# Optimization experiments

Measured on AMD Instinct MI355X. Metric: run time of the kernel, lower is better.

## Reference

```python
import jax, jax.numpy as jnp
import numpy as np

B, N = 32, 200000          # images, flattened candidates per image (anchors*classes)
NUM_CLASSES = 21           # VOC-style class count for the label-offset trick
CONF_THR = 0.05            # cfg.PRED_CONF_THR
NMS_THR = 0.5              # cfg.PRED_NMS_THR
TOPK = 500                 # cfg.PRED_SELECT_TOPK
KEEP_MAX = 100             # cfg.PRED_NMS_KEEP


def setup_inputs() -> dict:
    key = jax.random.key(0)
    k1, k2, k3, k4 = jax.random.split(key, 4)
    pscores = jax.random.uniform(k1, (B, N), dtype=jnp.float32)
    # well-formed ltrb boxes in [0,1]: right>left, bottom>top
    xy1 = jax.random.uniform(k2, (B, N, 2), dtype=jnp.float32) * 0.8
    wh = jax.random.uniform(k3, (B, N, 2), dtype=jnp.float32) * 0.2 + 0.01
    pboxes = jnp.concatenate([xy1, xy1 + wh], axis=-1)
    plabels = jax.random.randint(k4, (B, N), 0, NUM_CLASSES)
    return {"pscores": pscores, "pboxes": pboxes, "plabels": plabels}


def _box_iou(a, b):
    # a: [K,4], b: [K,4] ltrb -> [K,K] pairwise IoU (torchvision convention)
    lt = jnp.maximum(a[:, None, :2], b[None, :, :2])
    rb = jnp.minimum(a[:, None, 2:], b[None, :, 2:])
    wh = jnp.clip(rb - lt, 0.0)
    inter = wh[..., 0] * wh[..., 1]
    area_a = (a[:, 2] - a[:, 0]) * (a[:, 3] - a[:, 1])
    area_b = (b[:, 2] - b[:, 0]) * (b[:, 3] - b[:, 1])
    return inter / (area_a[:, None] + area_b[None, :] - inter)


def _greedy_nms(iou_mat, valid, thr):
    # candidates are pre-sorted by score descending (lax.top_k output order)
    K = valid.shape[0]
    idxs = jnp.arange(K)

    def body(keep, i):
        suppressed = jnp.any(keep & (iou_mat[i] > thr) & (idxs < i))
        k = valid[i] & (~suppressed)
        return keep.at[i].set(k), None

    keep, _ = jax.lax.scan(body, jnp.zeros((K,), dtype=bool), idxs)
    return keep


def reference(pscores, pboxes, plabels):
    # ---- threshold + top-k pre-selection (mask_pos AND mask_topk) ----
    scores_k, idx = jax.lax.top_k(pscores, TOPK)          # [B,K] sorted desc
    valid = scores_k > CONF_THR                           # equivalent to mask_pos & mask_topk
    bidx = jnp.arange(B)[:, None]
    boxes_k = pboxes[bidx, idx]                           # [B,K,4]
    labels_k = plabels[bidx, idx]                         # [B,K]

    # ---- multi-class NMS via label offset trick (batched_nms) ----
    max_coord = jnp.max(jnp.where(valid[..., None], boxes_k, 0.0), axis=(1, 2))  # [B]
    offsets = labels_k.astype(boxes_k.dtype) * (max_coord[:, None] + 1.0)
    boxes_nms = boxes_k + offsets[..., None]              # [B,K,4]

    iou = jax.vmap(_box_iou)(boxes_nms, boxes_nms)        # [B,K,K]
    keep = jax.vmap(lambda m, v: _greedy_nms(m, v, NMS_THR))(iou, valid)  # [B,K] bool

    # ---- keep[:num_max] per batch ----
    rank = jnp.cumsum(keep.astype(jnp.int32), axis=1)
    keep = keep & (rank <= KEEP_MAX)

    # compact kept entries to front (jnp.argsort is stable -> score order preserved), pad to KEEP_MAX
    order = jnp.argsort(jnp.where(keep, 0, 1), axis=1)[:, :KEEP_MAX]       # [B,KEEP]
    out_valid = jnp.take_along_axis(keep, order, axis=1)                    # [B,KEEP]
    boxes2 = jnp.take_along_axis(boxes_k, order[..., None], axis=1) * out_valid[..., None]
    scores2 = jnp.take_along_axis(scores_k, order, axis=1) * out_valid
    labels2 = jnp.where(out_valid, jnp.take_along_axis(labels_k, order, axis=1), -1)
    ids_batch2 = jnp.where(out_valid, jnp.arange(B)[:, None], -1)
    return ids_batch2, boxes2, labels2, scores2, out_valid
```

## Files before the change

kernel.cpp:

```cpp
#include <hip/hip_runtime.h>
#include <stdint.h>

#pragma clang fp contract(off)

#define BB 32
#define NN 200000
#define N4 50000
#define KK 500
#define KEEPN 100
#define CONF 0.05f
#define NMSTHR 0.5f
#define SLICES 8
#define SLICE_F4 6250
#define LBINS 8192
#define LSHIFT 19
#define LOCAL_CAP 2048
#define OUT_CAP 576
#define TMPCAP 640
#define OK0 0xBF733333u

typedef unsigned long long u64;


__device__ __forceinline__ unsigned int ordkey(float s) {
    unsigned int u = __float_as_uint(s);
    return (u & 0x80000000u) ? ~u : (u | 0x80000000u);
}

__device__ __forceinline__ void wappend(bool pred, u64 key, u64* keys, int* lcnt, int lane) {
    u64 bm = __ballot(pred);
    int pre = __popcll(bm & ((1ULL << lane) - 1ULL));
    int tt  = __popcll(bm);
    int base = 0;
    if (lane == 0 && tt > 0) base = atomicAdd(lcnt, tt);
    base = __shfl(base, 0);
    if (pred) { int pos = base + pre; if (pos < LOCAL_CAP) keys[pos] = key; }
}

__global__ __launch_bounds__(1024) void select_kernel(const float4* __restrict__ ps4,
                                                      u64* __restrict__ cand,
                                                      unsigned int* __restrict__ cnts) {
    __shared__ unsigned int hist[LBINS];
    __shared__ u64 keys[LOCAL_CAP];
    __shared__ unsigned int h[256];
    __shared__ unsigned int wsum[16];
    __shared__ u64 wmin[16], wmax[16];
    __shared__ u64 s_prefix;
    __shared__ unsigned int s_t13, s_region, s_cntgt;
    __shared__ int s_lcnt, s_sc, s_shift0;

    const int b = blockIdx.y, x = blockIdx.x;
    const int tid = threadIdx.x, lane = tid & 63, wv = tid >> 6;
    const float4* p = ps4 + (size_t)b * N4 + (size_t)x * SLICE_F4;
    const int ebase = x * (SLICE_F4 * 4);

    if (tid == 0) s_lcnt = 0;
    __syncthreads();

    for (int i = tid; i < SLICE_F4; i += 1024) {
        float4 v = p[i];
        int n = ebase + (i << 2);
        unsigned int ux = ordkey(v.x), uy = ordkey(v.y);
        unsigned int uz = ordkey(v.z), uw = ordkey(v.w);
        wappend(ux >= OK0, ((u64)ux << 32) | (unsigned int)(~(unsigned int)(n)),     keys, &s_lcnt, lane);
        wappend(uy >= OK0, ((u64)uy << 32) | (unsigned int)(~(unsigned int)(n + 1)), keys, &s_lcnt, lane);
        wappend(uz >= OK0, ((u64)uz << 32) | (unsigned int)(~(unsigned int)(n + 2)), keys, &s_lcnt, lane);
        wappend(uw >= OK0, ((u64)uw << 32) | (unsigned int)(~(unsigned int)(n + 3)), keys, &s_lcnt, lane);
    }
    __syncthreads();
    int m = s_lcnt;

    if (m < KK || m > LOCAL_CAP) {
        for (int i = tid; i < LBINS; i += 1024) hist[i] = 0;
        __syncthreads();
        for (int i = tid; i < SLICE_F4; i += 1024) {
            float4 v = p[i];
            atomicAdd(&hist[ordkey(v.x) >> LSHIFT], 1u);
            atomicAdd(&hist[ordkey(v.y) >> LSHIFT], 1u);
            atomicAdd(&hist[ordkey(v.z) >> LSHIFT], 1u);
            atomicAdd(&hist[ordkey(v.w) >> LSHIFT], 1u);
        }
        __syncthreads();
        unsigned int v8[8], tot = 0;
        for (int j = 0; j < 8; ++j) { v8[j] = hist[tid * 8 + j]; tot += v8[j]; }
        unsigned int sfx = tot;
        for (int off = 1; off < 64; off <<= 1) {
            unsigned int t2 = __shfl_down(sfx, off);
            sfx += (lane + off < 64) ? t2 : 0u;
        }
        if (lane == 0) wsum[wv] = sfx;
        __syncthreads();
        unsigned int wafter = 0;
        for (int w2 = wv + 1; w2 < 16; ++w2) wafter += wsum[w2];
        unsigned int sn = wafter + (sfx - tot);
        for (int j = 7; j >= 0; --j) {
            unsigned int s = sn + v8[j];
            if (s >= (unsigned)KK && sn < (unsigned)KK) s_t13 = (unsigned)(tid * 8 + j);
            sn = s;
        }
        if (tid == 0) s_lcnt = 0;
        __syncthreads();
        const unsigned int t13 = s_t13;
        for (int i = tid; i < SLICE_F4; i += 1024) {
            float4 v = p[i];
            int n = ebase + (i << 2);
            unsigned int u;
            u = ordkey(v.x); if ((u >> LSHIFT) >= t13) { int pos = atomicAdd(&s_lcnt, 1);
                if (pos < LOCAL_CAP) keys[pos] = ((u64)u << 32) | (unsigned int)(~(unsigned int)(n)); }
            u = ordkey(v.y); if ((u >> LSHIFT) >= t13) { int pos = atomicAdd(&s_lcnt, 1);
                if (pos < LOCAL_CAP) keys[pos] = ((u64)u << 32) | (unsigned int)(~(unsigned int)(n + 1)); }
            u = ordkey(v.z); if ((u >> LSHIFT) >= t13) { int pos = atomicAdd(&s_lcnt, 1);
                if (pos < LOCAL_CAP) keys[pos] = ((u64)u << 32) | (unsigned int)(~(unsigned int)(n + 2)); }
            u = ordkey(v.w); if ((u >> LSHIFT) >= t13) { int pos = atomicAdd(&s_lcnt, 1);
                if (pos < LOCAL_CAP) keys[pos] = ((u64)u << 32) | (unsigned int)(~(unsigned int)(n + 3)); }
        }
        __syncthreads();
        m = s_lcnt; if (m > LOCAL_CAP) m = LOCAL_CAP;
    }

    u64 thr; int seln;
    if (m <= OUT_CAP) {
        thr = 0ULL; seln = m;
    } else {
        u64 kmn = ~0ULL, kmx = 0ULL;
        for (int i = tid; i < m; i += 1024) {
            u64 k = keys[i];
            kmn = k < kmn ? k : kmn; kmx = k > kmx ? k : kmx;
        }
        for (int off = 32; off > 0; off >>= 1) {
            u64 a = __shfl_down(kmn, off), c = __shfl_down(kmx, off);
            if (lane + off < 64) { kmn = a < kmn ? a : kmn; kmx = c > kmx ? c : kmx; }
        }
        if (lane == 0) { wmin[wv] = kmn; wmax[wv] = kmx; }
        __syncthreads();
        if (tid == 0) {
            u64 mn = wmin[0], mx = wmax[0];
            for (int w2 = 1; w2 < 16; ++w2) {
                mn = wmin[w2] < mn ? wmin[w2] : mn;
                mx = wmax[w2] > mx ? wmax[w2] : mx;
            }
            u64 diff = mn ^ mx;
            int hb = 63 - __builtin_clzll(diff | 1ULL);
            int st = (hb >> 3) << 3;
            s_shift0 = st;
            s_prefix = (st == 56) ? 0ULL : (mx >> (st + 8));
            s_cntgt = 0u;
        }
        __syncthreads();
        int shift = s_shift0;
        for (; shift >= 0; shift -= 8) {
            if (tid < 256) h[tid] = 0u;
            __syncthreads();
            u64 pref = s_prefix;
            unsigned int cg = s_cntgt;
            for (int i = tid; i < m; i += 1024) {
                u64 k = keys[i];
                bool match = (shift == 56) || ((k >> (shift + 8)) == pref);
                if (match) atomicAdd(&h[(unsigned int)((k >> shift) & 0xFF)], 1u);
            }
            __syncthreads();
            if (wv == 0) {
                unsigned int b4[4]; unsigned int lt = 0;
                for (int j = 0; j < 4; ++j) { b4[j] = h[lane * 4 + j]; lt += b4[j]; }
                unsigned int sx = lt;
                for (int off = 1; off < 64; off <<= 1) {
                    unsigned int t2 = __shfl_down(sx, off);
                    sx += (lane + off < 64) ? t2 : 0u;
                }
                unsigned int after = sx - lt;
                unsigned int target = (unsigned)KK - cg;
                unsigned int sn2 = after;
                for (int j = 3; j >= 0; --j) {
                    unsigned int s = sn2 + b4[j];
                    if (s >= target && sn2 < target) {
                        unsigned int bin = (unsigned)(lane * 4 + j);
                        s_region = b4[j];
                        s_cntgt = cg + sn2;
                        s_prefix = (shift == 56) ? (u64)bin : ((pref << 8) | (u64)bin);
                    }
                    sn2 = s;
                }
            }
            __syncthreads();
            if (s_cntgt + s_region <= (unsigned)OUT_CAP) break;
        }
        if (shift < 0) shift = 0;
        thr = s_prefix << shift;
        seln = (int)(s_cntgt + s_region);
    }
    (void)seln;

    if (tid == 0) s_sc = 0;
    __syncthreads();
    u64* outslice = cand + (size_t)(b * SLICES + x) * OUT_CAP;
    for (int r0 = 0; r0 < LOCAL_CAP / 1024; ++r0) {
        int i = tid + r0 * 1024;
        u64 k = (i < m) ? keys[i] : 0ULL;
        bool pq = (i < m) && (k >= thr);
        u64 mb = __ballot(pq);
        int pre = __popcll(mb & ((1ULL << lane) - 1ULL));
        int tt = __popcll(mb);
        int base = 0;
        if (lane == 0 && tt > 0) base = atomicAdd(&s_sc, tt);
        base = __shfl(base, 0);
        if (pq && base + pre < OUT_CAP) outslice[base + pre] = k;
    }
    __syncthreads();
    if (tid == 0) {
        int c = s_sc; if (c > OUT_CAP) c = OUT_CAP;
        cnts[b * SLICES + x] = (unsigned)c;
    }
}

#define FITER 9
__global__ __launch_bounds__(512) void final_kernel(const float* __restrict__ pboxes,
                                                    const int* __restrict__ plabels,
                                                    const u64* __restrict__ cand,
                                                    const unsigned int* __restrict__ cnts,
                                                    float* __restrict__ out) {
    __shared__ u64 pool[4736];
    __shared__ float sboxes[KK * 5];
    __shared__ float sscore[KK];
    __shared__ int slabel[KK];
    __shared__ int clist[KK];
    __shared__ int scnt[SLICES];
    __shared__ int soff[SLICES + 1];
    __shared__ u64 wmin[8], wmax[8];
    __shared__ unsigned int wsum[8], wmaxh[8];
    __shared__ float wred[8];
    __shared__ int ccnt[21], coff[22], cfill[21];
    __shared__ u64 validw[8], sremv[8], s_km;
    __shared__ int kept[KEEPN];
    __shared__ u64 s_kmn, s_kmx, s_prefix;
    __shared__ unsigned int s_region, s_cntgt;
    __shared__ int s_shift, s_thrbin, s_selupper, s_fb, s_bsh, s_sc, s_nk, s_stop;
    __shared__ float s_maxc;

    unsigned int* hist = (unsigned int*)pool;
    unsigned int* pfx  = ((unsigned int*)pool) + 4096;
    u64* tmp = (u64*)((char*)pool + 32768);

    const int b = blockIdx.x;
    const int tid = threadIdx.x;
    const int lane = tid & 63;
    const int wv = tid >> 6;
    const u64* cb = cand + (size_t)b * SLICES * OUT_CAP;

    if (tid < SLICES) {
        int c = (int)cnts[b * SLICES + tid];
        scnt[tid] = c > OUT_CAP ? OUT_CAP : c;
    }
    if (tid == 0) { s_thrbin = 0; s_fb = 0; s_nk = 0; s_stop = 0; }
    __syncthreads();
    if (tid == 0) {
        int acc = 0;
        for (int s = 0; s < SLICES; ++s) { soff[s] = acc; acc += scnt[s]; }
        soff[SLICES] = acc;
    }
    __syncthreads();
    const int m = soff[SLICES];
    int so1 = soff[1], so2 = soff[2], so3 = soff[3], so4 = soff[4];
    int so5 = soff[5], so6 = soff[6], so7 = soff[7];

    for (int i = tid; i < 4096; i += 512) hist[i] = 0u;
    u64 kreg[FITER];
    u64 kmn = ~0ULL, kmx = 0ULL;
    #pragma unroll
    for (int r0 = 0; r0 < FITER; ++r0) {
        int i = tid + r0 * 512;
        u64 k = 0ULL;
        if (i < m) {
            int s = (i >= so1) + (i >= so2) + (i >= so3) + (i >= so4)
                  + (i >= so5) + (i >= so6) + (i >= so7);
            int base = (s == 0) ? 0 : soff[s];
            k = cb[(size_t)s * OUT_CAP + (i - base)];
            kmn = k < kmn ? k : kmn; kmx = k > kmx ? k : kmx;
        }
        kreg[r0] = k;
    }
    for (int off = 32; off > 0; off >>= 1) {
        u64 a = __shfl_down(kmn, off), c2 = __shfl_down(kmx, off);
        if (lane + off < 64) { kmn = a < kmn ? a : kmn; kmx = c2 > kmx ? c2 : kmx; }
    }
    if (lane == 0) { wmin[wv] = kmn; wmax[wv] = kmx; }
    __syncthreads();
    if (tid == 0) {
        u64 mn = wmin[0], mx = wmax[0];
        for (int w2 = 1; w2 < 8; ++w2) {
            mn = wmin[w2] < mn ? wmin[w2] : mn;
            mx = wmax[w2] > mx ? wmax[w2] : mx;
        }
        s_kmn = mn; s_kmx = mx;
        u64 diff = mn ^ mx;
        int hb = 63 - __builtin_clzll(diff | 1ULL);
        int sh = hb - 11; if (sh < 0) sh = 0;
        s_shift = sh;
    }
    __syncthreads();
    const int shift = s_shift;

    #pragma unroll
    for (int r0 = 0; r0 < FITER; ++r0) {
        int i = tid + r0 * 512;
        if (i < m) atomicAdd(&hist[(unsigned int)((kreg[r0] >> shift) & 0xFFFu)], 1u);
    }
    __syncthreads();

    unsigned int h8[8]; unsigned int lt = 0, hm = 0;
    const int g0 = tid << 3;
    #pragma unroll
    for (int j = 0; j < 8; ++j) { h8[j] = hist[g0 + j]; lt += h8[j]; hm = h8[j] > hm ? h8[j] : hm; }
    unsigned int sfx = lt;
    for (int off = 1; off < 64; off <<= 1) {
        unsigned int t2 = __shfl_down(sfx, off);
        sfx += (lane + off < 64) ? t2 : 0u;
    }
    unsigned int mh = hm;
    for (int off = 1; off < 64; off <<= 1) {
        unsigned int t2 = __shfl_down(mh, off);
        if (lane + off < 64) mh = t2 > mh ? t2 : mh;
    }
    if (lane == 0) { wsum[wv] = sfx; wmaxh[wv] = mh; }
    __syncthreads();
    unsigned int wafter = 0;
    for (int w2 = wv + 1; w2 < 8; ++w2) wafter += wsum[w2];
    unsigned int run = wafter + (sfx - lt);
    #pragma unroll
    for (int j = 7; j >= 0; --j) {
        pfx[g0 + j] = run;
        if (run < (unsigned)KK && run + h8[j] >= (unsigned)KK) s_thrbin = g0 + j;
        run += h8[j];
    }
    if (tid == 0) {
        unsigned int mmh = 0;
        for (int w2 = 0; w2 < 8; ++w2) mmh = wmaxh[w2] > mmh ? wmaxh[w2] : mmh;
        if (mmh > 64u) s_fb = 1;
    }
    __syncthreads();
    if (tid == 0) {
        int tb = s_thrbin;
        unsigned int su = pfx[tb] + hist[tb];
        s_selupper = (int)su;
        if (su > (unsigned)TMPCAP) s_fb = 1;
    }
    if (tid < KK) {
        sscore[tid] = -1.0f; slabel[tid] = 0;
        sboxes[tid * 5 + 0] = 0.0f; sboxes[tid * 5 + 1] = 0.0f;
        sboxes[tid * 5 + 2] = 0.0f; sboxes[tid * 5 + 3] = 0.0f;
    }
    __syncthreads();

    if (!s_fb) {
        const int thrbin = s_thrbin;
        #pragma unroll
        for (int r0 = 0; r0 < FITER; ++r0) {
            int i = tid + r0 * 512;
            if (i < m) {
                u64 k = kreg[r0];
                unsigned int g = (unsigned int)((k >> shift) & 0xFFFu);
                if ((int)g >= thrbin) {
                    unsigned int p = atomicAdd(&pfx[g], 1u);
                    if (p < (unsigned)TMPCAP) tmp[p] = k;
                }
            }
        }
        __syncthreads();
        int nr = s_selupper; if (nr > TMPCAP) nr = TMPCAP;
        for (int ii = tid; ii < nr; ii += 512) {
            u64 k = tmp[ii];
            unsigned int g = (unsigned int)((k >> shift) & 0xFFFu);
            unsigned int c = hist[g];
            unsigned int base = pfx[g] - c;
            unsigned int lo = (unsigned int)k, hi = (unsigned int)(k >> 32);
            int idx = (int)(~lo);
            unsigned int bits = (hi & 0x80000000u) ? (hi & 0x7FFFFFFFu) : ~hi;
            float msc = __uint_as_float(bits);
            const float4 bx = *(const float4*)(pboxes + (((size_t)b * NN + (size_t)idx) << 2));
            int lab = plabels[(size_t)b * NN + idx];
            int rank = 0;
            for (unsigned int q = 0; q < c; ++q) {
                u64 o = tmp[base + q];
                rank += (o > k) ? 1 : 0;
            }
            int fin = (int)base + rank;
            if (fin < KK) {
                sboxes[fin * 5 + 0] = bx.x; sboxes[fin * 5 + 1] = bx.y;
                sboxes[fin * 5 + 2] = bx.z; sboxes[fin * 5 + 3] = bx.w;
                sscore[fin] = msc; slabel[fin] = lab;
            }
        }
        __syncthreads();
    } else {
        if (tid == 0) {
            u64 mn = s_kmn, mx = s_kmx;
            u64 diff = mn ^ mx;
            int hb = 63 - __builtin_clzll(diff | 1ULL);
            int st = (hb >> 3) << 3;
            s_bsh = st;
            s_prefix = (st == 56) ? 0ULL : (mx >> (st + 8));
            s_cntgt = 0u;
        }
        __syncthreads();
        int sh2 = s_bsh;
        for (; sh2 >= 0; sh2 -= 8) {
            if (tid < 256) hist[tid] = 0u;
            __syncthreads();
            u64 pref = s_prefix;
            unsigned int cg = s_cntgt;
            #pragma unroll
            for (int r0 = 0; r0 < FITER; ++r0) {
                int i = tid + r0 * 512;
                if (i < m) {
                    u64 k = kreg[r0];
                    bool match = (sh2 == 56) || ((k >> (sh2 + 8)) == pref);
                    if (match) atomicAdd(&hist[(unsigned int)((k >> sh2) & 0xFF)], 1u);
                }
            }
            __syncthreads();
            if (wv == 0) {
                unsigned int b4[4]; unsigned int lt2 = 0;
                for (int j = 0; j < 4; ++j) { b4[j] = hist[lane * 4 + j]; lt2 += b4[j]; }
                unsigned int sx = lt2;
                for (int off = 1; off < 64; off <<= 1) {
                    unsigned int t2 = __shfl_down(sx, off);
                    sx += (lane + off < 64) ? t2 : 0u;
                }
                unsigned int after = sx - lt2;
                unsigned int target = (unsigned)KK - cg;
                unsigned int sn2 = after;
                for (int j = 3; j >= 0; --j) {
                    unsigned int s = sn2 + b4[j];
                    if (s >= target && sn2 < target) {
                        unsigned int bin = (unsigned)(lane * 4 + j);
                        s_region = b4[j];
                        s_cntgt = cg + sn2;
                        s_prefix = (sh2 == 56) ? (u64)bin : ((pref << 8) | (u64)bin);
                    }
                    sn2 = s;
                }
            }
            __syncthreads();
            if (s_cntgt + s_region <= (unsigned)OUT_CAP) break;
        }
        if (sh2 < 0) sh2 = 0;
        u64 thr2 = s_prefix << sh2;
        int seln = (int)(s_cntgt + s_region);
        if (seln > TMPCAP) seln = TMPCAP;
        if (tid == 0) s_sc = 0;
        __syncthreads();
        #pragma unroll
        for (int r0 = 0; r0 < FITER; ++r0) {
            int i = tid + r0 * 512;
            u64 k = (i < m) ? kreg[r0] : 0ULL;
            bool pq = (i < m) && (k >= thr2);
            u64 mb = __ballot(pq);
            int pre = __popcll(mb & ((1ULL << lane) - 1ULL));
            int tt = __popcll(mb);
            int bse = 0;
            if (lane == 0 && tt > 0) bse = atomicAdd(&s_sc, tt);
            bse = __shfl(bse, 0);
            if (pq) { int pos = bse + pre; if (pos < TMPCAP) tmp[pos] = k; }
        }
        __syncthreads();
        for (int r0 = 0; r0 < 2; ++r0) {
            int ii = tid + r0 * 512;
            if (ii - lane < seln) {
                u64 myk = (ii < seln) ? tmp[ii] : 0ULL;
                int r = 0;
                for (int base = 0; base < seln; base += 64) {
                    int i2 = base + lane;
                    u64 other = (i2 < seln) ? tmp[i2] : 0ULL;
                    unsigned int olo = (unsigned int)other, ohi = (unsigned int)(other >> 32);
                    int lim = seln - base; if (lim > 64) lim = 64;
                    for (int t2 = 0; t2 < lim; ++t2) {
                        unsigned int blo = (unsigned int)__builtin_amdgcn_readlane((int)olo, t2);
                        unsigned int bhi = (unsigned int)__builtin_amdgcn_readlane((int)ohi, t2);
                        u64 o = ((u64)bhi << 32) | (u64)blo;
                        r += (o > myk) ? 1 : 0;
                    }
                }
                if (ii < seln && r < KK) {
                    unsigned int lo = (unsigned int)myk, hi = (unsigned int)(myk >> 32);
                    int idx = (int)(~lo);
                    unsigned int bits = (hi & 0x80000000u) ? (hi & 0x7FFFFFFFu) : ~hi;
                    float msc = __uint_as_float(bits);
                    const float4 bx = *(const float4*)(pboxes + (((size_t)b * NN + (size_t)idx) << 2));
                    int lab = plabels[(size_t)b * NN + idx];
                    sboxes[r * 5 + 0] = bx.x; sboxes[r * 5 + 1] = bx.y;
                    sboxes[r * 5 + 2] = bx.z; sboxes[r * 5 + 3] = bx.w;
                    sscore[r] = msc; slabel[r] = lab;
                }
            }
        }
        __syncthreads();
    }

    float sc = (tid < KK) ? sscore[tid] : -1.0f;
    bool vq = (tid < KK) && (sc > CONF);
    u64 bm = __ballot(vq);
    if (lane == 0) validw[wv] = bm;
    float lm = vq ? fmaxf(fmaxf(sboxes[tid * 5 + 0], sboxes[tid * 5 + 1]),
                          fmaxf(sboxes[tid * 5 + 2], sboxes[tid * 5 + 3])) : 0.0f;
    for (int off = 32; off > 0; off >>= 1) lm = fmaxf(lm, __shfl_down(lm, off));
    if (lane == 0) wred[wv] = lm;
    __syncthreads();
    if (tid < 64) {
        float x = (tid < 8) ? wred[tid] : 0.0f;
        for (int off = 4; off > 0; off >>= 1) x = fmaxf(x, __shfl_down(x, off));
        if (tid == 0) s_maxc = x;
    }
    if (tid < 21) { ccnt[tid] = 0; cfill[tid] = 0; }
    if (tid < 8) sremv[tid] = 0ULL;
    __syncthreads();
    if (tid < KK) atomicAdd(&ccnt[slabel[tid]], 1);
    __syncthreads();
    if (tid == 0) {
        int acc = 0;
        for (int c = 0; c < 21; ++c) { coff[c] = acc; acc += ccnt[c]; }
        coff[21] = acc;
    }
    __syncthreads();
    if (tid < KK) {
        int c = slabel[tid];
        int pos = atomicAdd(&cfill[c], 1);
        clist[coff[c] + pos] = tid;
    }
    u64 (*msk)[512] = (u64(*)[512])pool;
    for (int i = tid; i < 8 * 512; i += 512) ((u64*)pool)[i] = 0ULL;
    __syncthreads();

    float ap1 = s_maxc + 1.0f;
    if (tid < KK) {
        int c = slabel[tid];
        int n = ccnt[c], base0 = coff[c];
        float aoff = (float)c * ap1;
        float a0 = sboxes[tid * 5 + 0] + aoff, a1 = sboxes[tid * 5 + 1] + aoff;
        float a2 = sboxes[tid * 5 + 2] + aoff, a3 = sboxes[tid * 5 + 3] + aoff;
        float areaA = (a2 - a0) * (a3 - a1);
        for (int q = 0; q < n; ++q) {
            int j = clist[base0 + q];
            float b0 = sboxes[j * 5 + 0] + aoff, b1f = sboxes[j * 5 + 1] + aoff;
            float b2f = sboxes[j * 5 + 2] + aoff, b3f = sboxes[j * 5 + 3] + aoff;
            float lt0 = fmaxf(a0, b0), lt1 = fmaxf(a1, b1f);
            float rb0 = fminf(a2, b2f), rb1 = fminf(a3, b3f);
            float ww = fmaxf(rb0 - lt0, 0.0f), hh = fmaxf(rb1 - lt1, 0.0f);
            float inter = ww * hh;
            float areaB = (b2f - b0) * (b3f - b1f);
            float iou = inter / (areaA + areaB - inter);
            if (iou > NMSTHR) msk[j >> 6][tid] |= (1ULL << (j & 63));
        }
    }
    __syncthreads();

    for (int c = 0; c < 8; ++c) {
        if (wv == 0) {
            u64 rowc = msk[c][c * 64 + lane];
            unsigned int rl = (unsigned int)rowc, rh = (unsigned int)(rowc >> 32);
            u64 cur = sremv[c];
            u64 vv = validw[c];
            u64 km = 0ULL;
            int nk = s_nk;
            for (int j = 0; j < 64; ++j) {
                if (nk >= KEEPN) break;
                bool alive = (((vv >> j) & 1ULL) != 0ULL) && (((cur >> j) & 1ULL) == 0ULL);
                if (alive) {
                    if (lane == 0) kept[nk] = c * 64 + j;
                    u64 rv = ((u64)(unsigned int)__builtin_amdgcn_readlane((int)rh, j) << 32)
                           |  (u64)(unsigned int)__builtin_amdgcn_readlane((int)rl, j);
                    cur |= rv;
                    km |= (1ULL << j);
                    ++nk;
                }
            }
            if (lane == 0) { s_km = km; s_nk = nk; sremv[c] = cur; s_stop = (nk >= KEEPN) ? 1 : 0; }
        }
        __syncthreads();
        if (s_stop || c == 7) break;
        if (wv > c) {
            u64 km = s_km;
            u64 v = ((km >> lane) & 1ULL) ? msk[wv][c * 64 + lane] : 0ULL;
            for (int off2 = 32; off2 > 0; off2 >>= 1) v |= __shfl_xor(v, off2);
            if (lane == 0) sremv[wv] |= v;
        }
        __syncthreads();
    }

    if (tid < KEEPN) {
        const int O_BOX = BB * KEEPN;
        const int O_LAB = BB * KEEPN * 5;
        const int O_SCO = BB * KEEPN * 6;
        const int O_VAL = BB * KEEPN * 7;
        bool q = tid < s_nk;
        int i = q ? kept[tid] : 0;
        int g = b * KEEPN + tid;
        out[g]                 = q ? (float)b : -1.0f;
        out[O_BOX + g * 4 + 0] = q ? sboxes[i * 5 + 0] : 0.0f;
        out[O_BOX + g * 4 + 1] = q ? sboxes[i * 5 + 1] : 0.0f;
        out[O_BOX + g * 4 + 2] = q ? sboxes[i * 5 + 2] : 0.0f;
        out[O_BOX + g * 4 + 3] = q ? sboxes[i * 5 + 3] : 0.0f;
        out[O_LAB + g]         = q ? (float)slabel[i] : -1.0f;
        out[O_SCO + g]         = q ? sscore[i] : 0.0f;
        out[O_VAL + g]         = q ? 1.0f : 0.0f;
    }
}

extern "C" void kernel_launch(void* const* d_in, const int* in_sizes, int n_in,
                              void* d_out, int out_size, void* d_ws, size_t ws_size,
                              hipStream_t stream) {
    const float* pscores = (const float*)d_in[0];
    const float* pboxes  = (const float*)d_in[1];
    const int*   plabels = (const int*)d_in[2];
    float* out = (float*)d_out;

    uint8_t* ws = (uint8_t*)d_ws;
    u64*          cand = (u64*)(ws + 0);
    unsigned int* cnts = (unsigned int*)(ws + 1179648);

    select_kernel<<<dim3(SLICES, BB), 1024, 0, stream>>>((const float4*)pscores, cand, cnts);
    final_kernel<<<BB, 512, 0, stream>>>(pboxes, plabels, cand, cnts, out);
}
```

Baseline: 196.9 us.

## Fuse select and final kernels with tagged inter-block flag handoff

```diff
diff --git a/kernel.cpp b/kernel.cpp
--- a/kernel.cpp
+++ b/kernel.cpp
@@ -18,6 +18,9 @@
 #define OUT_CAP 576
 #define TMPCAP 640
 #define OK0 0xBF733333u
+#define FITER 9
+#define TAG 0x5AB00000u
+#define TAGMASK 0xFFFFFC00u
 
 typedef unsigned long long u64;
 
@@ -37,192 +40,13 @@
     if (pred) { int pos = base + pre; if (pos < LOCAL_CAP) keys[pos] = key; }
 }
 
-__global__ __launch_bounds__(1024) void select_kernel(const float4* __restrict__ ps4,
-                                                      u64* __restrict__ cand,
-                                                      unsigned int* __restrict__ cnts) {
-    __shared__ unsigned int hist[LBINS];
-    __shared__ u64 keys[LOCAL_CAP];
-    __shared__ unsigned int h[256];
-    __shared__ unsigned int wsum[16];
-    __shared__ u64 wmin[16], wmax[16];
-    __shared__ u64 s_prefix;
-    __shared__ unsigned int s_t13, s_region, s_cntgt;
-    __shared__ int s_lcnt, s_sc, s_shift0;
-
-    const int b = blockIdx.y, x = blockIdx.x;
-    const int tid = threadIdx.x, lane = tid & 63, wv = tid >> 6;
-    const float4* p = ps4 + (size_t)b * N4 + (size_t)x * SLICE_F4;
-    const int ebase = x * (SLICE_F4 * 4);
-
-    if (tid == 0) s_lcnt = 0;
-    __syncthreads();
-
-    for (int i = tid; i < SLICE_F4; i += 1024) {
-        float4 v = p[i];
-        int n = ebase + (i << 2);
-        unsigned int ux = ordkey(v.x), uy = ordkey(v.y);
-        unsigned int uz = ordkey(v.z), uw = ordkey(v.w);
-        wappend(ux >= OK0, ((u64)ux << 32) | (unsigned int)(~(unsigned int)(n)),     keys, &s_lcnt, lane);
-        wappend(uy >= OK0, ((u64)uy << 32) | (unsigned int)(~(unsigned int)(n + 1)), keys, &s_lcnt, lane);
-        wappend(uz >= OK0, ((u64)uz << 32) | (unsigned int)(~(unsigned int)(n + 2)), keys, &s_lcnt, lane);
-        wappend(uw >= OK0, ((u64)uw << 32) | (unsigned int)(~(unsigned int)(n + 3)), keys, &s_lcnt, lane);
-    }
-    __syncthreads();
-    int m = s_lcnt;
-
-    if (m < KK || m > LOCAL_CAP) {
-        for (int i = tid; i < LBINS; i += 1024) hist[i] = 0;
-        __syncthreads();
-        for (int i = tid; i < SLICE_F4; i += 1024) {
-            float4 v = p[i];
-            atomicAdd(&hist[ordkey(v.x) >> LSHIFT], 1u);
-            atomicAdd(&hist[ordkey(v.y) >> LSHIFT], 1u);
-            atomicAdd(&hist[ordkey(v.z) >> LSHIFT], 1u);
-            atomicAdd(&hist[ordkey(v.w) >> LSHIFT], 1u);
-        }
-        __syncthreads();
-        unsigned int v8[8], tot = 0;
-        for (int j = 0; j < 8; ++j) { v8[j] = hist[tid * 8 + j]; tot += v8[j]; }
-        unsigned int sfx = tot;
-        for (int off = 1; off < 64; off <<= 1) {
-            unsigned int t2 = __shfl_down(sfx, off);
-            sfx += (lane + off < 64) ? t2 : 0u;
-        }
-        if (lane == 0) wsum[wv] = sfx;
-        __syncthreads();
-        unsigned int wafter = 0;
-        for (int w2 = wv + 1; w2 < 16; ++w2) wafter += wsum[w2];
-        unsigned int sn = wafter + (sfx - tot);
-        for (int j = 7; j >= 0; --j) {
-            unsigned int s = sn + v8[j];
-            if (s >= (unsigned)KK && sn < (unsigned)KK) s_t13 = (unsigned)(tid * 8 + j);
-            sn = s;
-        }
-        if (tid == 0) s_lcnt = 0;
-        __syncthreads();
-        const unsigned int t13 = s_t13;
-        for (int i = tid; i < SLICE_F4; i += 1024) {
-            float4 v = p[i];
-            int n = ebase + (i << 2);
-            unsigned int u;
-            u = ordkey(v.x); if ((u >> LSHIFT) >= t13) { int pos = atomicAdd(&s_lcnt, 1);
-                if (pos < LOCAL_CAP) keys[pos] = ((u64)u << 32) | (unsigned int)(~(unsigned int)(n)); }
-            u = ordkey(v.y); if ((u >> LSHIFT) >= t13) { int pos = atomicAdd(&s_lcnt, 1);
-                if (pos < LOCAL_CAP) keys[pos] = ((u64)u << 32) | (unsigned int)(~(unsigned int)(n + 1)); }
-            u = ordkey(v.z); if ((u >> LSHIFT) >= t13) { int pos = atomicAdd(&s_lcnt, 1);
-                if (pos < LOCAL_CAP) keys[pos] = ((u64)u << 32) | (unsigned int)(~(unsigned int)(n + 2)); }
-            u = ordkey(v.w); if ((u >> LSHIFT) >= t13) { int pos = atomicAdd(&s_lcnt, 1);
-                if (pos < LOCAL_CAP) keys[pos] = ((u64)u << 32) | (unsigned int)(~(unsigned int)(n + 3)); }
-        }
-        __syncthreads();
-        m = s_lcnt; if (m > LOCAL_CAP) m = LOCAL_CAP;
-    }
-
-    u64 thr; int seln;
-    if (m <= OUT_CAP) {
-        thr = 0ULL; seln = m;
-    } else {
-        u64 kmn = ~0ULL, kmx = 0ULL;
-        for (int i = tid; i < m; i += 1024) {
-            u64 k = keys[i];
-            kmn = k < kmn ? k : kmn; kmx = k > kmx ? k : kmx;
-        }
-        for (int off = 32; off > 0; off >>= 1) {
-            u64 a = __shfl_down(kmn, off), c = __shfl_down(kmx, off);
-            if (lane + off < 64) { kmn = a < kmn ? a : kmn; kmx = c > kmx ? c : kmx; }
-        }
-        if (lane == 0) { wmin[wv] = kmn; wmax[wv] = kmx; }
-        __syncthreads();
-        if (tid == 0) {
-            u64 mn = wmin[0], mx = wmax[0];
-            for (int w2 = 1; w2 < 16; ++w2) {
-                mn = wmin[w2] < mn ? wmin[w2] : mn;
-                mx = wmax[w2] > mx ? wmax[w2] : mx;
-            }
-            u64 diff = mn ^ mx;
-            int hb = 63 - __builtin_clzll(diff | 1ULL);
-            int st = (hb >> 3) << 3;
-            s_shift0 = st;
-            s_prefix = (st == 56) ? 0ULL : (mx >> (st + 8));
-            s_cntgt = 0u;
-        }
-        __syncthreads();
-        int shift = s_shift0;
-        for (; shift >= 0; shift -= 8) {
-            if (tid < 256) h[tid] = 0u;
-            __syncthreads();
-            u64 pref = s_prefix;
-            unsigned int cg = s_cntgt;
-            for (int i = tid; i < m; i += 1024) {
-                u64 k = keys[i];
-                bool match = (shift == 56) || ((k >> (shift + 8)) == pref);
-                if (match) atomicAdd(&h[(unsigned int)((k >> shift) & 0xFF)], 1u);
-            }
-            __syncthreads();
-            if (wv == 0) {
-                unsigned int b4[4]; unsigned int lt = 0;
-                for (int j = 0; j < 4; ++j) { b4[j] = h[lane * 4 + j]; lt += b4[j]; }
-                unsigned int sx = lt;
-                for (int off = 1; off < 64; off <<= 1) {
-                    unsigned int t2 = __shfl_down(sx, off);
-                    sx += (lane + off < 64) ? t2 : 0u;
-                }
-                unsigned int after = sx - lt;
-                unsigned int target = (unsigned)KK - cg;
-                unsigned int sn2 = after;
-                for (int j = 3; j >= 0; --j) {
-                    unsigned int s = sn2 + b4[j];
-                    if (s >= target && sn2 < target) {
-                        unsigned int bin = (unsigned)(lane * 4 + j);
-                        s_region = b4[j];
-                        s_cntgt = cg + sn2;
-                        s_prefix = (shift == 56) ? (u64)bin : ((pref << 8) | (u64)bin);
-                    }
-                    sn2 = s;
-                }
-            }
-            __syncthreads();
-            if (s_cntgt + s_region <= (unsigned)OUT_CAP) break;
-        }
-        if (shift < 0) shift = 0;
-        thr = s_prefix << shift;
-        seln = (int)(s_cntgt + s_region);
-    }
-    (void)seln;
-
-    if (tid == 0) s_sc = 0;
-    __syncthreads();
-    u64* outslice = cand + (size_t)(b * SLICES + x) * OUT_CAP;
-    for (int r0 = 0; r0 < LOCAL_CAP / 1024; ++r0) {
-        int i = tid + r0 * 1024;
-        u64 k = (i < m) ? keys[i] : 0ULL;
-        bool pq = (i < m) && (k >= thr);
-        u64 mb = __ballot(pq);
-        int pre = __popcll(mb & ((1ULL << lane) - 1ULL));
-        int tt = __popcll(mb);
-        int base = 0;
-        if (lane == 0 && tt > 0) base = atomicAdd(&s_sc, tt);
-        base = __shfl(base, 0);
-        if (pq && base + pre < OUT_CAP) outslice[base + pre] = k;
-    }
-    __syncthreads();
-    if (tid == 0) {
-        int c = s_sc; if (c > OUT_CAP) c = OUT_CAP;
-        cnts[b * SLICES + x] = (unsigned)c;
-    }
-}
-
-#define FITER 9
-__global__ __launch_bounds__(512) void final_kernel(const float* __restrict__ pboxes,
+__global__ __launch_bounds__(512) void fused_kernel(const float4* __restrict__ ps4,
+                                                    const float* __restrict__ pboxes,
                                                     const int* __restrict__ plabels,
-                                                    const u64* __restrict__ cand,
-                                                    const unsigned int* __restrict__ cnts,
+                                                    u64* cand,
+                                                    unsigned int* cnts,
                                                     float* __restrict__ out) {
-    __shared__ u64 pool[4736];
-    __shared__ float sboxes[KK * 5];
-    __shared__ float sscore[KK];
-    __shared__ int slabel[KK];
-    __shared__ int clist[KK];
+    __shared__ u64 smem[6736];
     __shared__ int scnt[SLICES];
     __shared__ int soff[SLICES + 1];
     __shared__ u64 wmin[8], wmax[8];
@@ -232,26 +56,202 @@
     __shared__ u64 validw[8], sremv[8], s_km;
     __shared__ int kept[KEEPN];
     __shared__ u64 s_kmn, s_kmx, s_prefix;
-    __shared__ unsigned int s_region, s_cntgt;
-    __shared__ int s_shift, s_thrbin, s_selupper, s_fb, s_bsh, s_sc, s_nk, s_stop;
+    __shared__ unsigned int s_region, s_cntgt, s_t13;
+    __shared__ int s_lcnt, s_sc, s_shift0, s_shift, s_thrbin, s_selupper, s_fb, s_bsh, s_nk, s_stop;
     __shared__ float s_maxc;
 
-    unsigned int* hist = (unsigned int*)pool;
-    unsigned int* pfx  = ((unsigned int*)pool) + 4096;
-    u64* tmp = (u64*)((char*)pool + 32768);
-
-    const int b = blockIdx.x;
-    const int tid = threadIdx.x;
-    const int lane = tid & 63;
-    const int wv = tid >> 6;
+    const int x = blockIdx.x, b = blockIdx.y;
+    const int tid = threadIdx.x, lane = tid & 63, wv = tid >> 6;
+
+    {
+        unsigned int* hist = (unsigned int*)smem;
+        u64* keys = (u64*)((char*)smem + 32768);
+        unsigned int* h256 = (unsigned int*)((char*)smem + 49152);
+        const float4* p = ps4 + (size_t)b * N4 + (size_t)x * SLICE_F4;
+        const int ebase = x * (SLICE_F4 * 4);
+
+        if (tid == 0) s_lcnt = 0;
+        __syncthreads();
+
+        for (int i = tid; i < SLICE_F4; i += 512) {
+            float4 v = p[i];
+            int n = ebase + (i << 2);
+            unsigned int ux = ordkey(v.x), uy = ordkey(v.y);
+            unsigned int uz = ordkey(v.z), uw = ordkey(v.w);
+            wappend(ux >= OK0, ((u64)ux << 32) | (unsigned int)(~(unsigned int)(n)),     keys, &s_lcnt, lane);
+            wappend(uy >= OK0, ((u64)uy << 32) | (unsigned int)(~(unsigned int)(n + 1)), keys, &s_lcnt, lane);
+            wappend(uz >= OK0, ((u64)uz << 32) | (unsigned int)(~(unsigned int)(n + 2)), keys, &s_lcnt, lane);
+            wappend(uw >= OK0, ((u64)uw << 32) | (unsigned int)(~(unsigned int)(n + 3)), keys, &s_lcnt, lane);
+        }
+        __syncthreads();
+        int m = s_lcnt;
+
+        if (m < KK || m > LOCAL_CAP) {
+            for (int i = tid; i < LBINS; i += 512) hist[i] = 0;
+            __syncthreads();
+            for (int i = tid; i < SLICE_F4; i += 512) {
+                float4 v = p[i];
+                atomicAdd(&hist[ordkey(v.x) >> LSHIFT], 1u);
+                atomicAdd(&hist[ordkey(v.y) >> LSHIFT], 1u);
+                atomicAdd(&hist[ordkey(v.z) >> LSHIFT], 1u);
+                atomicAdd(&hist[ordkey(v.w) >> LSHIFT], 1u);
+            }
+            __syncthreads();
+            unsigned int v16[16], tot = 0;
+            for (int j = 0; j < 16; ++j) { v16[j] = hist[tid * 16 + j]; tot += v16[j]; }
+            unsigned int sfx = tot;
+            for (int off = 1; off < 64; off <<= 1) {
+                unsigned int t2 = __shfl_down(sfx, off);
+                sfx += (lane + off < 64) ? t2 : 0u;
+            }
+            if (lane == 0) wsum[wv] = sfx;
+            __syncthreads();
+            unsigned int wafter = 0;
+            for (int w2 = wv + 1; w2 < 8; ++w2) wafter += wsum[w2];
+            unsigned int sn = wafter + (sfx - tot);
+            for (int j = 15; j >= 0; --j) {
+                unsigned int s = sn + v16[j];
+                if (s >= (unsigned)KK && sn < (unsigned)KK) s_t13 = (unsigned)(tid * 16 + j);
+                sn = s;
+            }
+            if (tid == 0) s_lcnt = 0;
+            __syncthreads();
+            const unsigned int t13 = s_t13;
+            for (int i = tid; i < SLICE_F4; i += 512) {
+                float4 v = p[i];
+                int n = ebase + (i << 2);
+                unsigned int u;
+                u = ordkey(v.x); if ((u >> LSHIFT) >= t13) { int pos = atomicAdd(&s_lcnt, 1);
+                    if (pos < LOCAL_CAP) keys[pos] = ((u64)u << 32) | (unsigned int)(~(unsigned int)(n)); }
+                u = ordkey(v.y); if ((u >> LSHIFT) >= t13) { int pos = atomicAdd(&s_lcnt, 1);
+                    if (pos < LOCAL_CAP) keys[pos] = ((u64)u << 32) | (unsigned int)(~(unsigned int)(n + 1)); }
+                u = ordkey(v.z); if ((u >> LSHIFT) >= t13) { int pos = atomicAdd(&s_lcnt, 1);
+                    if (pos < LOCAL_CAP) keys[pos] = ((u64)u << 32) | (unsigned int)(~(unsigned int)(n + 2)); }
+                u = ordkey(v.w); if ((u >> LSHIFT) >= t13) { int pos = atomicAdd(&s_lcnt, 1);
+                    if (pos < LOCAL_CAP) keys[pos] = ((u64)u << 32) | (unsigned int)(~(unsigned int)(n + 3)); }
+            }
+            __syncthreads();
+            m = s_lcnt; if (m > LOCAL_CAP) m = LOCAL_CAP;
+        }
+
+        u64 thr;
+        if (m <= OUT_CAP) {
+            thr = 0ULL;
+        } else {
+            u64 kmn = ~0ULL, kmx = 0ULL;
+            for (int i = tid; i < m; i += 512) {
+                u64 k = keys[i];
+                kmn = k < kmn ? k : kmn; kmx = k > kmx ? k : kmx;
+            }
+            for (int off = 32; off > 0; off >>= 1) {
+                u64 a = __shfl_down(kmn, off), c = __shfl_down(kmx, off);
+                if (lane + off < 64) { kmn = a < kmn ? a : kmn; kmx = c > kmx ? c : kmx; }
+            }
+            if (lane == 0) { wmin[wv] = kmn; wmax[wv] = kmx; }
+            __syncthreads();
+            if (tid == 0) {
+                u64 mn = wmin[0], mx = wmax[0];
+                for (int w2 = 1; w2 < 8; ++w2) {
+                    mn = wmin[w2] < mn ? wmin[w2] : mn;
+                    mx = wmax[w2] > mx ? wmax[w2] : mx;
+                }
+                u64 diff = mn ^ mx;
+                int hb = 63 - __builtin_clzll(diff | 1ULL);
+                int st = (hb >> 3) << 3;
+                s_shift0 = st;
+                s_prefix = (st == 56) ? 0ULL : (mx >> (st + 8));
+                s_cntgt = 0u;
+            }
+            __syncthreads();
+            int shift = s_shift0;
+            for (; shift >= 0; shift -= 8) {
+                if (tid < 256) h256[tid] = 0u;
+                __syncthreads();
+                u64 pref = s_prefix;
+                unsigned int cg = s_cntgt;
+                for (int i = tid; i < m; i += 512) {
+                    u64 k = keys[i];
+                    bool match = (shift == 56) || ((k >> (shift + 8)) == pref);
+                    if (match) atomicAdd(&h256[(unsigned int)((k >> shift) & 0xFF)], 1u);
+                }
+                __syncthreads();
+                if (wv == 0) {
+                    unsigned int b4[4]; unsigned int lt = 0;
+                    for (int j = 0; j < 4; ++j) { b4[j] = h256[lane * 4 + j]; lt += b4[j]; }
+                    unsigned int sx = lt;
+                    for (int off = 1; off < 64; off <<= 1) {
+                        unsigned int t2 = __shfl_down(sx, off);
+                        sx += (lane + off < 64) ? t2 : 0u;
+                    }
+                    unsigned int after = sx - lt;
+                    unsigned int target = (unsigned)KK - cg;
+                    unsigned int sn2 = after;
+                    for (int j = 3; j >= 0; --j) {
+                        unsigned int s = sn2 + b4[j];
+                        if (s >= target && sn2 < target) {
+                            unsigned int bin = (unsigned)(lane * 4 + j);
+                            s_region = b4[j];
+                            s_cntgt = cg + sn2;
+                            s_prefix = (shift == 56) ? (u64)bin : ((pref << 8) | (u64)bin);
+                        }
+                        sn2 = s;
+                    }
+                }
+                __syncthreads();
+                if (s_cntgt + s_region <= (unsigned)OUT_CAP) break;
+            }
+            if (shift < 0) shift = 0;
+            thr = s_prefix << shift;
+        }
+
+        if (tid == 0) s_sc = 0;
+        __syncthreads();
+        u64* outslice = cand + (size_t)(b * SLICES + x) * OUT_CAP;
+        for (int r0 = 0; r0 < LOCAL_CAP / 512; ++r0) {
+            int i = tid + r0 * 512;
+            u64 k = (i < m) ? keys[i] : 0ULL;
+            bool pq = (i < m) && (k >= thr);
+            u64 mb = __ballot(pq);
+            int pre = __popcll(mb & ((1ULL << lane) - 1ULL));
+            int tt = __popcll(mb);
+            int base = 0;
+            if (lane == 0 && tt > 0) base = atomicAdd(&s_sc, tt);
+            base = __shfl(base, 0);
+            if (pq && base + pre < OUT_CAP) outslice[base + pre] = k;
+        }
+        __syncthreads();
+        if (tid == 0) {
+            int c = s_sc; if (c > OUT_CAP) c = OUT_CAP;
+            __threadfence();
+            __hip_atomic_store(&cnts[b * SLICES + x], TAG | (unsigned int)c,
+                               __ATOMIC_RELAXED, __HIP_MEMORY_SCOPE_AGENT);
+        }
+    }
+    if (x != 0) return;
+
+    unsigned int* fhist = (unsigned int*)smem;
+    unsigned int* pfx   = ((unsigned int*)smem) + 4096;
+    u64* tmp = (u64*)((char*)smem + 32768);
+    float* sboxes = (float*)((char*)smem + 37888);
+    float* sscore = (float*)((char*)smem + 47888);
+    int* slabel = (int*)((char*)smem + 49888);
+    int* clist  = (int*)((char*)smem + 51888);
     const u64* cb = cand + (size_t)b * SLICES * OUT_CAP;
 
     if (tid < SLICES) {
-        int c = (int)cnts[b * SLICES + tid];
-        scnt[tid] = c > OUT_CAP ? OUT_CAP : c;
+        const unsigned int* cp = cnts + b * SLICES + tid;
+        unsigned int v;
+        for (;;) {
+            v = __hip_atomic_load(cp, __ATOMIC_RELAXED, __HIP_MEMORY_SCOPE_AGENT);
+            if ((v & TAGMASK) == TAG) break;
+            __builtin_amdgcn_s_sleep(1);
+        }
+        int c = (int)(v & 0x3FFu); if (c > OUT_CAP) c = OUT_CAP;
+        scnt[tid] = c;
     }
     if (tid == 0) { s_thrbin = 0; s_fb = 0; s_nk = 0; s_stop = 0; }
     __syncthreads();
+    __threadfence();
     if (tid == 0) {
         int acc = 0;
         for (int s = 0; s < SLICES; ++s) { soff[s] = acc; acc += scnt[s]; }
@@ -262,7 +262,7 @@
     int so1 = soff[1], so2 = soff[2], so3 = soff[3], so4 = soff[4];
     int so5 = soff[5], so6 = soff[6], so7 = soff[7];
 
-    for (int i = tid; i < 4096; i += 512) hist[i] = 0u;
+    for (int i = tid; i < 4096; i += 512) fhist[i] = 0u;
     u64 kreg[FITER];
     u64 kmn = ~0ULL, kmx = 0ULL;
     #pragma unroll
@@ -302,14 +302,14 @@
     #pragma unroll
     for (int r0 = 0; r0 < FITER; ++r0) {
         int i = tid + r0 * 512;
-        if (i < m) atomicAdd(&hist[(unsigned int)((kreg[r0] >> shift) & 0xFFFu)], 1u);
+        if (i < m) atomicAdd(&fhist[(unsigned int)((kreg[r0] >> shift) & 0xFFFu)], 1u);
     }
     __syncthreads();
 
     unsigned int h8[8]; unsigned int lt = 0, hm = 0;
     const int g0 = tid << 3;
     #pragma unroll
-    for (int j = 0; j < 8; ++j) { h8[j] = hist[g0 + j]; lt += h8[j]; hm = h8[j] > hm ? h8[j] : hm; }
+    for (int j = 0; j < 8; ++j) { h8[j] = fhist[g0 + j]; lt += h8[j]; hm = h8[j] > hm ? h8[j] : hm; }
     unsigned int sfx = lt;
     for (int off = 1; off < 64; off <<= 1) {
         unsigned int t2 = __shfl_down(sfx, off);
@@ -339,7 +339,7 @@
     __syncthreads();
     if (tid == 0) {
         int tb = s_thrbin;
-        unsigned int su = pfx[tb] + hist[tb];
+        unsigned int su = pfx[tb] + fhist[tb];
         s_selupper = (int)su;
         if (su > (unsigned)TMPCAP) s_fb = 1;
     }
@@ -369,7 +369,7 @@
         for (int ii = tid; ii < nr; ii += 512) {
             u64 k = tmp[ii];
             unsigned int g = (unsigned int)((k >> shift) & 0xFFFu);
-            unsigned int c = hist[g];
+            unsigned int c = fhist[g];
             unsigned int base = pfx[g] - c;
             unsigned int lo = (unsigned int)k, hi = (unsigned int)(k >> 32);
             int idx = (int)(~lo);
@@ -403,7 +403,7 @@
         __syncthreads();
         int sh2 = s_bsh;
         for (; sh2 >= 0; sh2 -= 8) {
-            if (tid < 256) hist[tid] = 0u;
+            if (tid < 256) fhist[tid] = 0u;
             __syncthreads();
             u64 pref = s_prefix;
             unsigned int cg = s_cntgt;
@@ -413,13 +413,13 @@
                 if (i < m) {
                     u64 k = kreg[r0];
                     bool match = (sh2 == 56) || ((k >> (sh2 + 8)) == pref);
-                    if (match) atomicAdd(&hist[(unsigned int)((k >> sh2) & 0xFF)], 1u);
+                    if (match) atomicAdd(&fhist[(unsigned int)((k >> sh2) & 0xFF)], 1u);
                 }
             }
             __syncthreads();
             if (wv == 0) {
                 unsigned int b4[4]; unsigned int lt2 = 0;
-                for (int j = 0; j < 4; ++j) { b4[j] = hist[lane * 4 + j]; lt2 += b4[j]; }
+                for (int j = 0; j < 4; ++j) { b4[j] = fhist[lane * 4 + j]; lt2 += b4[j]; }
                 unsigned int sx = lt2;
                 for (int off = 1; off < 64; off <<= 1) {
                     unsigned int t2 = __shfl_down(sx, off);
@@ -505,9 +505,9 @@
     if (lane == 0) wred[wv] = lm;
     __syncthreads();
     if (tid < 64) {
-        float x = (tid < 8) ? wred[tid] : 0.0f;
-        for (int off = 4; off > 0; off >>= 1) x = fmaxf(x, __shfl_down(x, off));
-        if (tid == 0) s_maxc = x;
+        float xx = (tid < 8) ? wred[tid] : 0.0f;
+        for (int off = 4; off > 0; off >>= 1) xx = fmaxf(xx, __shfl_down(xx, off));
+        if (tid == 0) s_maxc = xx;
     }
     if (tid < 21) { ccnt[tid] = 0; cfill[tid] = 0; }
     if (tid < 8) sremv[tid] = 0ULL;
@@ -525,8 +525,8 @@
         int pos = atomicAdd(&cfill[c], 1);
         clist[coff[c] + pos] = tid;
     }
-    u64 (*msk)[512] = (u64(*)[512])pool;
-    for (int i = tid; i < 8 * 512; i += 512) ((u64*)pool)[i] = 0ULL;
+    u64 (*msk)[512] = (u64(*)[512])smem;
+    for (int i = tid; i < 8 * 512; i += 512) ((u64*)smem)[i] = 0ULL;
     __syncthreads();
 
     float ap1 = s_maxc + 1.0f;
@@ -602,6 +602,8 @@
         out[O_SCO + g]         = q ? sscore[i] : 0.0f;
         out[O_VAL + g]         = q ? 1.0f : 0.0f;
     }
+
+    if (tid < SLICES) cnts[b * SLICES + tid] = 0u;
 }
 
 extern "C" void kernel_launch(void* const* d_in, const int* in_sizes, int n_in,
@@ -616,6 +618,6 @@
     u64*          cand = (u64*)(ws + 0);
     unsigned int* cnts = (unsigned int*)(ws + 1179648);
 
-    select_kernel<<<dim3(SLICES, BB), 1024, 0, stream>>>((const float4*)pscores, cand, cnts);
-    final_kernel<<<BB, 512, 0, stream>>>(pboxes, plabels, cand, cnts, out);
+    fused_kernel<<<dim3(SLICES, BB), 512, 0, stream>>>((const float4*)pscores, pboxes,
+                                                       plabels, cand, cnts, out);
 }
```

After: 235.6 us. 1.2x slower.
